# Kernel tuning notes

Hardware: AMD Instinct MI355X
Metric: run time of the kernel (lower is better)

The kernel has to match this reference:

```python
import jax, jax.numpy as jnp
import numpy as np

B, L, H, C, K, S = 32, 512, 336, 321, 8, 8   # batch, seq_len, pred_len, channels, leaders, states
FREQ = H // 2 + 1                            # 169
G = 2 * K + 1                                # filter groups
TEMP = 1.0
EPS = 1e-5


def setup_inputs() -> dict:
    key = jax.random.key(0)
    ks = jax.random.split(key, 12)
    x = jax.random.normal(ks[0], (B, L, C), jnp.float32)
    leader_ids = jax.random.randint(ks[1], (B, C, K), 0, C)
    shift = jax.random.randint(ks[2], (B, C, K), 0, L)
    r = jax.random.normal(ks[3], (B, C, K), jnp.float32)
    # backbone linear: seq_len -> pred_len
    Wb = jax.random.normal(ks[4], (H, L), jnp.float32) * float(1.0 / np.sqrt(L))
    bb = jnp.zeros((H,), jnp.float32)
    # factory classifier: (L + K) features -> state_num logits
    Wc = jax.random.normal(ks[5], (S, L + K), jnp.float32) * float(1.0 / np.sqrt(L + K))
    bc = jnp.zeros((S,), jnp.float32)
    # state prototype filters (complex, stored as re/im): [S, 2K+1, FREQ]
    states_re = jax.random.normal(ks[6], (S, G, FREQ), jnp.float32) * float(1.0 / np.sqrt(S))
    states_im = jax.random.normal(ks[7], (S, G, FREQ), jnp.float32) * float(1.0 / np.sqrt(S))
    # complex mix layer: 3*FREQ -> FREQ
    Wm_re = jax.random.normal(ks[8], (FREQ, 3 * FREQ), jnp.float32) * float(1.0 / np.sqrt(3 * FREQ))
    Wm_im = jax.random.normal(ks[9], (FREQ, 3 * FREQ), jnp.float32) * float(1.0 / np.sqrt(3 * FREQ))
    bm_re = jnp.zeros((FREQ,), jnp.float32)
    bm_im = jnp.zeros((FREQ,), jnp.float32)
    return dict(x=x, r=r, Wb=Wb, bb=bb, Wc=Wc, bc=bc,
                states_re=states_re, states_im=states_im,
                Wm_re=Wm_re, Wm_im=Wm_im, bm_re=bm_re, bm_im=bm_im,
                leader_ids=leader_ids, shift=shift)


def reference(x, r, Wb, bb, Wc, bc, states_re, states_im, Wm_re, Wm_im, bm_re, bm_im, leader_ids, shift):
    xc = jnp.transpose(x, (0, 2, 1))                      # [B,C,L]
    mu = xc.mean(-1, keepdims=True)
    norm = jnp.sqrt(xc.var(-1, keepdims=True) + EPS)
    xn = (xc - mu) / norm                                 # instance_norm
    y_hat = jnp.einsum('bcl,hl->bch', xn, Wb) + bb        # backbone [B,C,H]

    # --- shifted_leader_seq (torch.no_grad) ---
    full = jax.lax.stop_gradient(jnp.concatenate([xn, y_hat], -1))      # [B,C,L+H]
    lead_full = full[jnp.arange(B)[:, None, None], leader_ids]          # [B,C,K,L+H]
    t_idx = (L - shift)[..., None] + jnp.arange(H)                      # [B,C,K,H]
    seq_shifted = jnp.take_along_axis(lead_full, t_idx, axis=-1)        # [B,C,K,H]
    r = jax.lax.stop_gradient(r)

    # softmax leader weights with leading constant-one slot
    ones = jnp.ones((B, C, 1), xn.dtype)
    r_soft = jax.nn.softmax(jnp.concatenate([ones, jnp.abs(r)], -1) / TEMP, axis=-1)  # [B,C,K+1]

    # --- factory: state-mixed complex filters ---
    feat = jnp.concatenate([xn, r_soft[..., 1:]], -1)                   # [B,C,L+K]
    p = jax.nn.softmax(jnp.einsum('bcf,sf->bcs', feat, Wc) + bc, axis=-1)
    states = states_re + 1j * states_im                                 # [S,G,FREQ]
    filters = jnp.einsum('bcs,sgf->bcgf', p, states)                    # [B,C,2K+1,FREQ]

    # --- FFT filter multiply-sum + inverse FFT mix ---
    y_hat_f = jnp.fft.rfft(y_hat)                                       # [B,C,FREQ]
    seq_shifted_f = jnp.fft.rfft(seq_shifted) * filters[:, :, :K]       # [B,C,K,FREQ]
    seq_diff_f = (seq_shifted_f - y_hat_f[:, :, None]) * filters[:, :, K:-1]
    yh_f = y_hat_f * filters[:, :, -1]
    z = jnp.concatenate([seq_shifted_f.sum(2), seq_diff_f.sum(2), yh_f], -1)  # [B,C,3*FREQ]
    Wm = Wm_re + 1j * Wm_im
    mixed = jnp.einsum('bcf,gf->bcg', z, Wm) + (bm_re + 1j * bm_im)     # [B,C,FREQ]
    y_hat = y_hat + jnp.fft.irfft(mixed, n=H)

    y = y_hat * norm + mu
    return jnp.transpose(y, (0, 2, 1))                                  # [B,H,C]
```

## Files before the change

kernel.cpp:

```cpp
#include <hip/hip_runtime.h>
#include <math.h>

#define B_ 32
#define L_ 512
#define H_ 336
#define C_ 321
#define K_ 8
#define S_ 8
#define FREQ_ 169
#define G_ 17
#define LHB_ 848
#define F_FEAT 520
#define EPS_ 1e-5f
#define BCN_ (B_ * C_)
#define NROW_ (BCN_ * 9)
#define NROWP_ 92480
#define ZNBC_ 8

#ifndef M_PIf
#define M_PIf 3.14159265358979323846f
#endif

typedef __attribute__((ext_vector_type(8))) short short8v;
typedef __attribute__((ext_vector_type(4))) float f32x4;

__device__ __forceinline__ unsigned short f2bf(float x) {
    unsigned u = __builtin_bit_cast(unsigned, x);
    u += 0x7FFFu + ((u >> 16) & 1u);
    return (unsigned short)(u >> 16);
}
__device__ __forceinline__ float bf2f(unsigned short h) {
    return __builtin_bit_cast(float, (unsigned)h << 16);
}


__global__ void k_prep_dft(unsigned short* __restrict__ T) {
    int blk = blockIdx.x, kc = blk / 22, nt = blk % 22, lane = threadIdx.x;
    int n = nt * 16 + (lane & 15);
    int kb = kc * 32 + (lane >> 4) * 8;
    int f = n >> 1;
    unsigned short* dst = T + (size_t)blk * 512 + lane * 8;
    for (int i = 0; i < 8; ++i) {
        int k = kb + i;
        float val = 0.f;
        if (k < H_ && n < 2 * FREQ_) {
            int m = (k * f) % H_;
            float s, c;
            sincosf((float)m * (2.0f * M_PIf / (float)H_), &s, &c);
            val = (n & 1) ? -s : c;
        }
        dst[i] = f2bf(val);
    }
}

__global__ __launch_bounds__(256) void k_prep_tab(float* __restrict__ ctb,
                                                  float* __restrict__ stb) {
    int idx = blockIdx.x * 256 + threadIdx.x;
    if (idx >= FREQ_ * H_) return;
    int g = idx / H_, h = idx % H_;
    int m = (g * h) % H_;
    float s, c;
    sincosf((float)m * (2.0f * M_PIf / (float)H_), &s, &c);
    float wgt = ((g == 0 || g == FREQ_ - 1) ? 1.0f : 2.0f) * (1.0f / (float)H_);
    ctb[idx] = wgt * c;
    stb[idx] = -wgt * s;
}

__global__ __launch_bounds__(256) void k_prep_wt3(const float* __restrict__ Wm_re,
                                                  const float* __restrict__ Wm_im,
                                                  const float* __restrict__ ctb,
                                                  const float* __restrict__ stb,
                                                  unsigned short* __restrict__ T) {
    int t = blockIdx.x * 256 + threadIdx.x;
    if (t >= 512 * H_) return;
    int k = t / H_, h = t - k * H_;
    float s1 = 0.f, s2 = 0.f;
    if (k < 3 * FREQ_) {
        #pragma unroll 4
        for (int g = 0; g < FREQ_; ++g) {
            float ct = ctb[g * H_ + h];
            float st = stb[g * H_ + h];
            float wr = Wm_re[(size_t)g * (3 * FREQ_) + k];
            float wi = Wm_im[(size_t)g * (3 * FREQ_) + k];
            s1 += wr * ct + wi * st;
            s2 += wr * st - wi * ct;
        }
    }
    int nt = h >> 4, nr = h & 15;
    {
        int kc = k >> 5, kr = k & 31;
        int lane = ((kr >> 3) << 4) | nr;
        T[((size_t)(kc * 21 + nt)) * 512 + lane * 8 + (k & 7)] = f2bf(s1);
    }
    {
        int kk = k + 512;
        int kc = kk >> 5, kr = kk & 31;
        int lane = ((kr >> 3) << 4) | nr;
        T[((size_t)(kc * 21 + nt)) * 512 + lane * 8 + (kk & 7)] = f2bf(s2);
    }
}

__global__ __launch_bounds__(64) void k_prep_bv(const float* __restrict__ bm_re,
                                                const float* __restrict__ bm_im,
                                                const float* __restrict__ ctb,
                                                const float* __restrict__ stb,
                                                float* __restrict__ bvec) {
    int h = blockIdx.x * 64 + threadIdx.x;
    if (h >= H_) return;
    float acc = 0.f;
    for (int g = 0; g < FREQ_; ++g)
        acc += bm_re[g] * ctb[g * H_ + h] + bm_im[g] * stb[g * H_ + h];
    bvec[h] = acc;
}

__global__ void k_prep_wb(const float* __restrict__ Wb, unsigned short* __restrict__ T) {
    int blk = blockIdx.x, kc = blk / 21, nt = blk % 21, lane = threadIdx.x;
    int n = nt * 16 + (lane & 15);
    int kb = kc * 32 + (lane >> 4) * 8;
    unsigned short* dst = T + (size_t)blk * 512 + lane * 8;
    for (int i = 0; i < 8; ++i) {
        int k = kb + i;
        dst[i] = f2bf(Wb[(size_t)n * L_ + k]);
    }
}

__global__ __launch_bounds__(256) void k_prep_st2(const float* __restrict__ st_re,
                                                  const float* __restrict__ st_im,
                                                  float4* __restrict__ stf4,
                                                  float2* __restrict__ stg3) {
    int idx = blockIdx.x * 256 + threadIdx.x;
    if (idx < 64 * FREQ_) {
        int row = idx / FREQ_, f = idx % FREQ_;
        int k = row >> 3, s = row & 7;
        size_t b1 = (size_t)s * (G_ * FREQ_) + (size_t)k * FREQ_ + f;
        size_t b2 = (size_t)s * (G_ * FREQ_) + (size_t)(8 + k) * FREQ_ + f;
        stf4[idx] = make_float4(st_re[b1], st_im[b1], st_re[b2], st_im[b2]);
    }
    if (idx < 8 * FREQ_) {
        int s = idx / FREQ_, f = idx % FREQ_;
        size_t b3 = (size_t)s * (G_ * FREQ_) + (size_t)16 * FREQ_ + f;
        stg3[idx] = make_float2(st_re[b3], st_im[b3]);
    }
}

__global__ __launch_bounds__(256) void k_stats_part(const float* __restrict__ x,
                                                    float2* __restrict__ part) {
    __shared__ float red_s[4][64], red_q[4][64];
    int tid = threadIdx.x, w = tid >> 6, lane = tid & 63;
    int b = blockIdx.y, c0 = blockIdx.x * 64, l0 = blockIdx.z * 64;
    int c = c0 + lane;
    bool valid = (c < C_);
    const float* xb = x + ((size_t)b * L_) * C_;
    float s = 0.f, q = 0.f;
    for (int li = w; li < 64; li += 4) {
        float v = valid ? xb[(size_t)(l0 + li) * C_ + c] : 0.f;
        s += v; q += v * v;
    }
    red_s[w][lane] = s; red_q[w][lane] = q;
    __syncthreads();
    if (w == 0) {
        float S = red_s[0][lane] + red_s[1][lane] + red_s[2][lane] + red_s[3][lane];
        float Q = red_q[0][lane] + red_q[1][lane] + red_q[2][lane] + red_q[3][lane];
        part[(size_t)(((b * 6 + blockIdx.x) * 8) + blockIdx.z) * 64 + lane] = make_float2(S, Q);
    }
}

__global__ __launch_bounds__(256) void k_stats_fin(const float2* __restrict__ part,
                                                   float* __restrict__ muv,
                                                   float* __restrict__ nrm) {
    int t = blockIdx.x * 256 + threadIdx.x;
    int b = t / 384, rem = t % 384;
    int ct = rem / 64, cl = rem % 64;
    int c = ct * 64 + cl;
    if (b >= B_ || c >= C_) return;
    float S = 0.f, Q = 0.f;
    #pragma unroll
    for (int ls = 0; ls < 8; ++ls) {
        float2 p = part[(size_t)(((b * 6 + ct) * 8) + ls) * 64 + cl];
        S += p.x; Q += p.y;
    }
    float mu = S / (float)L_;
    float var = Q / (float)L_ - mu * mu;
    float n = sqrtf(var + EPS_);
    muv[(size_t)b * C_ + c] = mu;
    nrm[(size_t)b * C_ + c] = n;
}

__global__ __launch_bounds__(256) void k_norm(const float* __restrict__ x,
                                              const float* __restrict__ muv,
                                              const float* __restrict__ nrm,
                                              unsigned short* __restrict__ fullbf) {
    __shared__ float tl[64][65];
    int tid = threadIdx.x, w = tid >> 6, lane = tid & 63;
    int b = blockIdx.y, c0 = blockIdx.x * 64, l0 = blockIdx.z * 64;
    int c = c0 + lane;
    bool valid = (c < C_);
    const float* xb = x + ((size_t)b * L_) * C_;
    float mu = valid ? muv[(size_t)b * C_ + c] : 0.f;
    float inv = valid ? (1.0f / nrm[(size_t)b * C_ + c]) : 0.f;
    for (int li = w; li < 64; li += 4) {
        float v = valid ? xb[(size_t)(l0 + li) * C_ + c] : 0.f;
        tl[li][lane] = (v - mu) * inv;
    }
    __syncthreads();
    for (int cr = w; cr < 64; cr += 4) {
        int cc = c0 + cr;
        if (cc < C_ && lane < 32) {
            size_t bc = (size_t)b * C_ + cc;
            unsigned pk = (unsigned)f2bf(tl[2 * lane][cr]) |
                          ((unsigned)f2bf(tl[2 * lane + 1][cr]) << 16);
            ((unsigned*)fullbf)[(bc * LHB_ + l0) / 2 + lane] = pk;
        }
    }
}

__global__ __launch_bounds__(256) void k_yhat(const unsigned short* __restrict__ fullbf_r,
                                              const unsigned short* __restrict__ Wbsw,
                                              const float* __restrict__ bb,
                                              unsigned short* __restrict__ fullbf_w,
                                              float* __restrict__ yhf) {
    int bc0 = blockIdx.x * 32;
    int half = blockIdx.y;
    int tid = threadIdx.x, w = tid >> 6, lane = tid & 63;
    const int NTB0[5] = {0, 3, 6, 9, 11};
    const int NTB1[5] = {11, 14, 17, 19, 21};
    int nt0 = half ? NTB1[w] : NTB0[w];
    int ntn = (half ? NTB1[w + 1] : NTB0[w + 1]) - nt0;
    int r15 = lane & 15, kg = lane >> 4;
    f32x4 acc[2][3];
    #pragma unroll
    for (int mf = 0; mf < 2; ++mf)
        #pragma unroll
        for (int j = 0; j < 3; ++j) acc[mf][j] = (f32x4){0.f, 0.f, 0.f, 0.f};
    for (int kc = 0; kc < 16; ++kc) {
        short8v a[2];
        #pragma unroll
        for (int mf = 0; mf < 2; ++mf)
            a[mf] = *(const short8v*)(fullbf_r + ((size_t)(bc0 + mf * 16 + r15) * LHB_ + kc * 32 + kg * 8));
        #pragma unroll
        for (int j = 0; j < 3; ++j) {
            if (j >= ntn) continue;
            short8v bfr = *(const short8v*)(Wbsw + ((size_t)(kc * 21 + nt0 + j) * 512 + lane * 8));
            #pragma unroll
            for (int mf = 0; mf < 2; ++mf)
                acc[mf][j] = __builtin_amdgcn_mfma_f32_16x16x32_bf16(a[mf], bfr, acc[mf][j], 0, 0, 0);
        }
    }
    #pragma unroll
    for (int mf = 0; mf < 2; ++mf)
        #pragma unroll
        for (int j = 0; j < 3; ++j) {
            if (j >= ntn) continue;
            int n_ = (nt0 + j) * 16 + r15;
            #pragma unroll
            for (int reg = 0; reg < 4; ++reg) {
                int bc = bc0 + mf * 16 + kg * 4 + reg;
                float v = acc[mf][j][reg] + bb[n_];
                fullbf_w[(size_t)bc * LHB_ + L_ + n_] = f2bf(v);
                yhf[(size_t)bc * H_ + n_] = v;
            }
        }
}

__global__ __launch_bounds__(256) void k_p2(const unsigned short* __restrict__ fullbf,
                                            const float* __restrict__ r,
                                            const float* __restrict__ Wc,
                                            const float* __restrict__ bcv,
                                            float* __restrict__ p_out) {
    __shared__ float WcS[8 * F_FEAT];
    __shared__ float rsS[16][8];
    __shared__ float bcS[8];
    int tid = threadIdx.x, w = tid >> 6, lane = tid & 63;
    int bc0 = blockIdx.x * 16;
    for (int i = tid; i < 8 * F_FEAT; i += 256) WcS[i] = Wc[i];
    if (tid < 8) bcS[tid] = bcv[tid];
    if (tid < 16) {
        int bc = bc0 + tid;
        const float* rr = r + (size_t)bc * K_;
        float a[8]; float m = 1.0f;
        #pragma unroll
        for (int k = 0; k < 8; ++k) { a[k] = fabsf(rr[k]); m = fmaxf(m, a[k]); }
        float Z = expf(1.0f - m);
        float e[8];
        #pragma unroll
        for (int k = 0; k < 8; ++k) { e[k] = expf(a[k] - m); Z += e[k]; }
        float inv = 1.0f / Z;
        #pragma unroll
        for (int k = 0; k < 8; ++k) rsS[tid][k] = e[k] * inv;
    }
    __syncthreads();

    for (int i = 0; i < 4; ++i) {
        int bcl = w * 4 + i;
        int bc = bc0 + bcl;
        const unsigned* xrow = (const unsigned*)(fullbf + (size_t)bc * LHB_);
        float acc[8] = {0.f, 0.f, 0.f, 0.f, 0.f, 0.f, 0.f, 0.f};
        #pragma unroll
        for (int t = 0; t < 4; ++t) {
            int j = lane + t * 64;
            unsigned v = xrow[j];
            float x0 = bf2f((unsigned short)(v & 0xffff));
            float x1 = bf2f((unsigned short)(v >> 16));
            #pragma unroll
            for (int s = 0; s < 8; ++s)
                acc[s] += x0 * WcS[s * F_FEAT + 2 * j] + x1 * WcS[s * F_FEAT + 2 * j + 1];
        }
        if (lane < 8) {
            float xf = rsS[bcl][lane];
            #pragma unroll
            for (int s = 0; s < 8; ++s) acc[s] += xf * WcS[s * F_FEAT + L_ + lane];
        }
        #pragma unroll
        for (int s = 0; s < 8; ++s) {
            #pragma unroll
            for (int off = 32; off > 0; off >>= 1) acc[s] += __shfl_down(acc[s], off);
        }
        if (lane == 0) {
            float m = -1e30f;
            #pragma unroll
            for (int s = 0; s < 8; ++s) { acc[s] += bcS[s]; m = fmaxf(m, acc[s]); }
            float Z = 0.f; float e[8];
            #pragma unroll
            for (int s = 0; s < 8; ++s) { e[s] = expf(acc[s] - m); Z += e[s]; }
            float inv = 1.0f / Z;
            #pragma unroll
            for (int s = 0; s < 8; ++s) p_out[(size_t)bc * 8 + s] = e[s] * inv;
        }
    }
}

__global__ __launch_bounds__(512) void k_dft3(const unsigned short* __restrict__ fullbf,
                                              const int* __restrict__ leader,
                                              const int* __restrict__ shiftp,
                                              const unsigned short* __restrict__ Tsw,
                                              unsigned short* __restrict__ Xbf) {
    __shared__ unsigned short A[64 * 360];
    int tid = threadIdx.x, w = tid >> 6, lane = tid & 63;
    int row0 = blockIdx.x * 64;

    #pragma unroll
    for (int i = 0; i < 8; ++i) {
        int rr = w * 8 + i;
        int r = row0 + rr;
        unsigned short* dst = A + rr * 360;
        if (r < NROW_) {
            int bc = r / 9, k = r - bc * 9;
            int b = bc / C_;
            const unsigned short* src;
            if (k < 8) {
                int lead = leader[(size_t)bc * K_ + k];
                int sh = shiftp[(size_t)bc * K_ + k];
                src = fullbf + ((size_t)b * C_ + lead) * LHB_ + (L_ - sh);
            } else {
                src = fullbf + (size_t)bc * LHB_ + L_;
            }
            #pragma unroll
            for (int t = 0; t < 6; ++t) {
                int j = lane + t * 64;
                if (j < 352) dst[j] = (j < H_) ? src[j] : (unsigned short)0;
            }
        } else {
            #pragma unroll
            for (int t = 0; t < 6; ++t) {
                int j = lane + t * 64;
                if (j < 352) dst[j] = 0;
            }
        }
    }
    __syncthreads();

    const int NTB[9] = {0, 3, 6, 9, 11, 14, 17, 20, 22};
    int nt0 = NTB[w], ntn = NTB[w + 1] - nt0;
    int r15 = lane & 15, kg = lane >> 4;
    f32x4 acc[4][3];
    #pragma unroll
    for (int mf = 0; mf < 4; ++mf)
        #pragma unroll
        for (int j = 0; j < 3; ++j) acc[mf][j] = (f32x4){0.f, 0.f, 0.f, 0.f};
    for (int kc = 0; kc < 11; ++kc) {
        short8v a[4];
        #pragma unroll
        for (int mf = 0; mf < 4; ++mf)
            a[mf] = *(const short8v*)(A + (size_t)(mf * 16 + r15) * 360 + kc * 32 + kg * 8);
        #pragma unroll
        for (int j = 0; j < 3; ++j) {
            if (j >= ntn) continue;
            short8v bfr = *(const short8v*)(Tsw + ((size_t)(kc * 22 + nt0 + j) * 512 + lane * 8));
            #pragma unroll
            for (int mf = 0; mf < 4; ++mf)
                acc[mf][j] = __builtin_amdgcn_mfma_f32_16x16x32_bf16(a[mf], bfr, acc[mf][j], 0, 0, 0);
        }
    }
    #pragma unroll
    for (int mf = 0; mf < 4; ++mf)
        #pragma unroll
        for (int j = 0; j < 3; ++j) {
            if (j >= ntn) continue;
            int col = (nt0 + j) * 16 + r15;
            #pragma unroll
            for (int reg = 0; reg < 4; ++reg) {
                int row = row0 + mf * 16 + kg * 4 + reg;
                Xbf[(size_t)row * 352 + col] = f2bf(acc[mf][j][reg]);
            }
        }
}

__global__ __launch_bounds__(256) void k_z3(const unsigned* __restrict__ X32,
                                            const float* __restrict__ pbuf,
                                            const float4* __restrict__ stf4,
                                            const float2* __restrict__ stg3,
                                            unsigned short* __restrict__ zbf) {
    __shared__ float psL[ZNBC_][8];
    int tid = threadIdx.x;
    int bc0 = blockIdx.x * ZNBC_;
    if (tid < ZNBC_ * 8) {
        int bcl = tid >> 3, s = tid & 7;
        psL[bcl][s] = pbuf[(size_t)(bc0 + bcl) * 8 + s];
    }
    __syncthreads();

    if (tid < FREQ_) {
        int f = tid;
        float z1r[ZNBC_], z1i[ZNBC_], z2r[ZNBC_], z2i[ZNBC_], Yr[ZNBC_], Yi[ZNBC_];
        #pragma unroll
        for (int bcl = 0; bcl < ZNBC_; ++bcl) {
            z1r[bcl] = z1i[bcl] = z2r[bcl] = z2i[bcl] = 0.f;
            unsigned v = X32[((size_t)(bc0 + bcl) * 9 + 8) * 176 + f];
            Yr[bcl] = bf2f((unsigned short)(v & 0xffff));
            Yi[bcl] = bf2f((unsigned short)(v >> 16));
        }
        for (int k = 0; k < 8; ++k) {
            float4 stv[8];
            #pragma unroll
            for (int s = 0; s < 8; ++s) stv[s] = stf4[(size_t)(k * 8 + s) * FREQ_ + f];
            #pragma unroll
            for (int bcl = 0; bcl < ZNBC_; ++bcl) {
                float f1r = 0.f, f1i = 0.f, f2r = 0.f, f2i = 0.f;
                #pragma unroll
                for (int s = 0; s < 8; ++s) {
                    float p = psL[bcl][s];
                    f1r += p * stv[s].x; f1i += p * stv[s].y;
                    f2r += p * stv[s].z; f2i += p * stv[s].w;
                }
                unsigned v = X32[((size_t)(bc0 + bcl) * 9 + k) * 176 + f];
                float Xr = bf2f((unsigned short)(v & 0xffff));
                float Xi = bf2f((unsigned short)(v >> 16));
                float ar = Xr * f1r - Xi * f1i;
                float ai = Xr * f1i + Xi * f1r;
                z1r[bcl] += ar; z1i[bcl] += ai;
                float dr = ar - Yr[bcl], di = ai - Yi[bcl];
                z2r[bcl] += dr * f2r - di * f2i;
                z2i[bcl] += dr * f2i + di * f2r;
            }
        }
        #pragma unroll
        for (int bcl = 0; bcl < ZNBC_; ++bcl) {
            int bc = bc0 + bcl;
            float f3r = 0.f, f3i = 0.f;
            #pragma unroll
            for (int s = 0; s < 8; ++s) {
                float2 v3 = stg3[(size_t)s * FREQ_ + f];
                float p = psL[bcl][s];
                f3r += p * v3.x; f3i += p * v3.y;
            }
            unsigned short* zrow = zbf + (size_t)bc * 1024;
            zrow[f]       = f2bf(z1r[bcl]);  zrow[512 + f]       = f2bf(z1i[bcl]);
            zrow[169 + f] = f2bf(z2r[bcl]);  zrow[512 + 169 + f] = f2bf(z2i[bcl]);
            zrow[338 + f] = f2bf(Yr[bcl] * f3r - Yi[bcl] * f3i);
            zrow[512 + 338 + f] = f2bf(Yr[bcl] * f3i + Yi[bcl] * f3r);
        }
    } else if (tid >= 176 && tid < 176 + ZNBC_ * 10) {
        int t = tid - 176;
        int bcl = t / 10, o = t - bcl * 10;
        unsigned short* zrow = zbf + (size_t)(bc0 + bcl) * 1024;
        if (o < 5) zrow[507 + o] = 0;
        else       zrow[1019 + (o - 5)] = 0;
    }
}

__global__ __launch_bounds__(256) void k_mixf(const unsigned short* __restrict__ zbf,
                                              const unsigned short* __restrict__ WTsw,
                                              const float* __restrict__ bvec,
                                              const float* __restrict__ yhf,
                                              const float* __restrict__ muv,
                                              const float* __restrict__ nrm,
                                              float* __restrict__ ytmp) {
    int bc0 = blockIdx.x * 32;
    int half = blockIdx.y;
    int tid = threadIdx.x, w = tid >> 6, lane = tid & 63;
    const int NTB0[5] = {0, 3, 6, 9, 11};
    const int NTB1[5] = {11, 14, 17, 19, 21};
    int nt0 = half ? NTB1[w] : NTB0[w];
    int ntn = (half ? NTB1[w + 1] : NTB0[w + 1]) - nt0;
    int r15 = lane & 15, kg = lane >> 4;
    f32x4 acc[2][3];
    #pragma unroll
    for (int mf = 0; mf < 2; ++mf)
        #pragma unroll
        for (int j = 0; j < 3; ++j) acc[mf][j] = (f32x4){0.f, 0.f, 0.f, 0.f};
    for (int kc = 0; kc < 32; ++kc) {
        short8v a[2];
        #pragma unroll
        for (int mf = 0; mf < 2; ++mf)
            a[mf] = *(const short8v*)(zbf + ((size_t)(bc0 + mf * 16 + r15) * 1024 + kc * 32 + kg * 8));
        #pragma unroll
        for (int j = 0; j < 3; ++j) {
            if (j >= ntn) continue;
            short8v bfr = *(const short8v*)(WTsw + ((size_t)(kc * 21 + nt0 + j) * 512 + lane * 8));
            #pragma unroll
            for (int mf = 0; mf < 2; ++mf)
                acc[mf][j] = __builtin_amdgcn_mfma_f32_16x16x32_bf16(a[mf], bfr, acc[mf][j], 0, 0, 0);
        }
    }
    #pragma unroll
    for (int mf = 0; mf < 2; ++mf)
        #pragma unroll
        for (int j = 0; j < 3; ++j) {
            if (j >= ntn) continue;
            int h = (nt0 + j) * 16 + r15;
            float bv = bvec[h];
            #pragma unroll
            for (int reg = 0; reg < 4; ++reg) {
                int bc = bc0 + mf * 16 + kg * 4 + reg;
                float y = (yhf[(size_t)bc * H_ + h] + acc[mf][j][reg] + bv) * nrm[bc] + muv[bc];
                ytmp[(size_t)bc * H_ + h] = y;
            }
        }
}

__global__ __launch_bounds__(256) void k_out_t(const float* __restrict__ ytmp,
                                               float* __restrict__ out) {
    __shared__ float tile[32][33];
    int b = blockIdx.z;
    int h0 = blockIdx.x * 32, c0 = blockIdx.y * 32;
    int tx = threadIdx.x & 31, ty = threadIdx.x >> 5;
    #pragma unroll
    for (int i = 0; i < 4; ++i) {
        int cc = c0 + ty + i * 8, hh = h0 + tx;
        if (cc < C_ && hh < H_)
            tile[ty + i * 8][tx] = ytmp[((size_t)b * C_ + cc) * H_ + hh];
    }
    __syncthreads();
    #pragma unroll
    for (int i = 0; i < 4; ++i) {
        int hh = h0 + ty + i * 8, cc = c0 + tx;
        if (cc < C_ && hh < H_)
            out[((size_t)b * H_ + hh) * C_ + cc] = tile[tx][ty + i * 8];
    }
}

extern "C" void kernel_launch(void* const* d_in, const int* in_sizes, int n_in,
                              void* d_out, int out_size, void* d_ws, size_t ws_size,
                              hipStream_t stream) {
    const float* x     = (const float*)d_in[0];
    const float* r     = (const float*)d_in[1];
    const float* Wb    = (const float*)d_in[2];
    const float* bb    = (const float*)d_in[3];
    const float* Wc    = (const float*)d_in[4];
    const float* bcv   = (const float*)d_in[5];
    const float* st_re = (const float*)d_in[6];
    const float* st_im = (const float*)d_in[7];
    const float* Wm_re = (const float*)d_in[8];
    const float* Wm_im = (const float*)d_in[9];
    const float* bm_re = (const float*)d_in[10];
    const float* bm_im = (const float*)d_in[11];
    const int* leader  = (const int*)d_in[12];
    const int* shiftp  = (const int*)d_in[13];
    float* out = (float*)d_out;

    char* w = (char*)d_ws;
    auto carve = [&](size_t bytes) {
        char* p = w;
        w += (bytes + 255) & ~(size_t)255;
        return (void*)p;
    };
    unsigned short* Tdft = (unsigned short*)carve((size_t)11 * 22 * 512 * 2);
    unsigned short* WTsw = (unsigned short*)carve((size_t)32 * 21 * 512 * 2);
    unsigned short* Wbsw = (unsigned short*)carve((size_t)16 * 21 * 512 * 2);
    float*          ctb  = (float*)carve((size_t)FREQ_ * H_ * 4);
    float*          stb  = (float*)carve((size_t)FREQ_ * H_ * 4);
    float*          bvec = (float*)carve((size_t)H_ * 4);
    float4*         stf4 = (float4*)carve((size_t)64 * FREQ_ * 16);
    float2*         stg3 = (float2*)carve((size_t)8 * FREQ_ * 8);
    float2*         part = (float2*)carve((size_t)B_ * 6 * 8 * 64 * 8);
    unsigned short* fullbf = (unsigned short*)carve((size_t)BCN_ * LHB_ * 2);
    float*          yhf  = (float*)carve((size_t)BCN_ * H_ * 4);
    float*          muv  = (float*)carve((size_t)BCN_ * 4);
    float*          nrm  = (float*)carve((size_t)BCN_ * 4);
    float*          pbuf = (float*)carve((size_t)BCN_ * 8 * 4);
    unsigned short* zbf  = (unsigned short*)carve((size_t)BCN_ * 1024 * 2);
    float*          ytmp = (float*)carve((size_t)BCN_ * H_ * 4);
    unsigned short* Xbf  = (unsigned short*)carve((size_t)NROWP_ * 352 * 2);

    hipLaunchKernelGGL(k_prep_dft, dim3(11 * 22), dim3(64), 0, stream, Tdft);
    hipLaunchKernelGGL(k_prep_tab, dim3((FREQ_ * H_ + 255) / 256), dim3(256), 0, stream, ctb, stb);
    hipLaunchKernelGGL(k_prep_wt3, dim3((512 * H_ + 255) / 256), dim3(256), 0, stream,
                       Wm_re, Wm_im, ctb, stb, WTsw);
    hipLaunchKernelGGL(k_prep_bv,  dim3((H_ + 63) / 64), dim3(64), 0, stream, bm_re, bm_im, ctb, stb, bvec);
    hipLaunchKernelGGL(k_prep_wb,  dim3(16 * 21), dim3(64), 0, stream, Wb, Wbsw);
    hipLaunchKernelGGL(k_prep_st2, dim3((64 * FREQ_ + 255) / 256), dim3(256), 0, stream,
                       st_re, st_im, stf4, stg3);
    hipLaunchKernelGGL(k_stats_part, dim3(6, 32, 8), dim3(256), 0, stream, x, part);
    hipLaunchKernelGGL(k_stats_fin, dim3(48), dim3(256), 0, stream, part, muv, nrm);
    hipLaunchKernelGGL(k_norm, dim3(6, 32, 8), dim3(256), 0, stream, x, muv, nrm, fullbf);
    hipLaunchKernelGGL(k_yhat, dim3(BCN_ / 32, 2), dim3(256), 0, stream, fullbf, Wbsw, bb, fullbf, yhf);
    hipLaunchKernelGGL(k_p2, dim3(BCN_ / 16), dim3(256), 0, stream, fullbf, r, Wc, bcv, pbuf);
    hipLaunchKernelGGL(k_dft3, dim3(NROWP_ / 64), dim3(512), 0, stream,
                       fullbf, leader, shiftp, Tdft, Xbf);
    hipLaunchKernelGGL(k_z3, dim3(BCN_ / ZNBC_), dim3(256), 0, stream,
                       (const unsigned*)Xbf, pbuf, stf4, stg3, zbf);
    hipLaunchKernelGGL(k_mixf, dim3(BCN_ / 32, 2), dim3(256), 0, stream,
                       zbf, WTsw, bvec, yhf, muv, nrm, ytmp);
    hipLaunchKernelGGL(k_out_t, dim3((H_ + 31) / 32, (C_ + 31) / 32, B_), dim3(256), 0, stream,
                       ytmp, out);
}
```

Measured before the change: 258.0 us.

## Fuse DFT with filter-mix stage and fold output transpose into mix kernel

Merges the batched DFT GEMM with the z-computation so spectra stay in shared memory instead of round-tripping through a large global Xbf buffer. Each block now handles 7 (b,c) pairs, which gives 63 of 64 rows and wastes one MFMA row. The separate transpose kernel is removed: the mix kernel stages results in a shared tile and writes the transposed output directly. These changes cut global traffic and launches, at the cost of more shared memory per block and output writes that are strided across channels.

```diff
diff --git a/kernel.cpp b/kernel.cpp
--- a/kernel.cpp
+++ b/kernel.cpp
@@ -13,9 +13,7 @@
 #define F_FEAT 520
 #define EPS_ 1e-5f
 #define BCN_ (B_ * C_)
-#define NROW_ (BCN_ * 9)
-#define NROWP_ 92480
-#define ZNBC_ 8
+#define DZB_ 7
 
 #ifndef M_PIf
 #define M_PIf 3.14159265358979323846f
@@ -329,22 +327,34 @@
     }
 }
 
-__global__ __launch_bounds__(512) void k_dft3(const unsigned short* __restrict__ fullbf,
-                                              const int* __restrict__ leader,
-                                              const int* __restrict__ shiftp,
-                                              const unsigned short* __restrict__ Tsw,
-                                              unsigned short* __restrict__ Xbf) {
+__global__ __launch_bounds__(512) void k_dftz2(const unsigned short* __restrict__ fullbf,
+                                               const int* __restrict__ leader,
+                                               const int* __restrict__ shiftp,
+                                               const unsigned short* __restrict__ Tsw,
+                                               const float* __restrict__ pbuf,
+                                               const float4* __restrict__ stf4,
+                                               const float2* __restrict__ stg3,
+                                               unsigned short* __restrict__ zbf) {
     __shared__ unsigned short A[64 * 360];
+    __shared__ float psL[DZB_][8];
     int tid = threadIdx.x, w = tid >> 6, lane = tid & 63;
-    int row0 = blockIdx.x * 64;
+    int bc0 = blockIdx.x * DZB_;
+    unsigned* A32 = (unsigned*)A;
+    for (int i = tid; i < 64 * 180; i += 512) A32[i] = 0;
+    if (tid < DZB_ * 8) {
+        int bcl = tid >> 3, s = tid & 7;
+        int bc = bc0 + bcl;
+        psL[bcl][s] = (bc < BCN_) ? pbuf[(size_t)bc * 8 + s] : 0.f;
+    }
+    __syncthreads();
 
     #pragma unroll
     for (int i = 0; i < 8; ++i) {
         int rr = w * 8 + i;
-        int r = row0 + rr;
-        unsigned short* dst = A + rr * 360;
-        if (r < NROW_) {
-            int bc = r / 9, k = r - bc * 9;
+        if (rr >= 63) break;
+        int bcl = rr / 9, k = rr - bcl * 9;
+        int bc = bc0 + bcl;
+        if (bc < BCN_) {
             int b = bc / C_;
             const unsigned short* src;
             if (k < 8) {
@@ -354,16 +364,11 @@
             } else {
                 src = fullbf + (size_t)bc * LHB_ + L_;
             }
+            unsigned short* dst = A + rr * 360;
             #pragma unroll
             for (int t = 0; t < 6; ++t) {
                 int j = lane + t * 64;
-                if (j < 352) dst[j] = (j < H_) ? src[j] : (unsigned short)0;
-            }
-        } else {
-            #pragma unroll
-            for (int t = 0; t < 6; ++t) {
-                int j = lane + t * 64;
-                if (j < 352) dst[j] = 0;
+                if (j < H_) dst[j] = src[j];
             }
         }
     }
@@ -391,6 +396,8 @@
                 acc[mf][j] = __builtin_amdgcn_mfma_f32_16x16x32_bf16(a[mf], bfr, acc[mf][j], 0, 0, 0);
         }
     }
+    __syncthreads();
+
     #pragma unroll
     for (int mf = 0; mf < 4; ++mf)
         #pragma unroll
@@ -399,42 +406,34 @@
             int col = (nt0 + j) * 16 + r15;
             #pragma unroll
             for (int reg = 0; reg < 4; ++reg) {
-                int row = row0 + mf * 16 + kg * 4 + reg;
-                Xbf[(size_t)row * 352 + col] = f2bf(acc[mf][j][reg]);
+                int row = mf * 16 + kg * 4 + reg;
+                A[row * 360 + col] = f2bf(acc[mf][j][reg]);
             }
         }
-}
-
-__global__ __launch_bounds__(256) void k_z3(const unsigned* __restrict__ X32,
-                                            const float* __restrict__ pbuf,
-                                            const float4* __restrict__ stf4,
-                                            const float2* __restrict__ stg3,
-                                            unsigned short* __restrict__ zbf) {
-    __shared__ float psL[ZNBC_][8];
-    int tid = threadIdx.x;
-    int bc0 = blockIdx.x * ZNBC_;
-    if (tid < ZNBC_ * 8) {
-        int bcl = tid >> 3, s = tid & 7;
-        psL[bcl][s] = pbuf[(size_t)(bc0 + bcl) * 8 + s];
-    }
-    __syncthreads();
-
-    if (tid < FREQ_) {
-        int f = tid;
-        float z1r[ZNBC_], z1i[ZNBC_], z2r[ZNBC_], z2i[ZNBC_], Yr[ZNBC_], Yi[ZNBC_];
-        #pragma unroll
-        for (int bcl = 0; bcl < ZNBC_; ++bcl) {
-            z1r[bcl] = z1i[bcl] = z2r[bcl] = z2i[bcl] = 0.f;
-            unsigned v = X32[((size_t)(bc0 + bcl) * 9 + 8) * 176 + f];
-            Yr[bcl] = bf2f((unsigned short)(v & 0xffff));
-            Yi[bcl] = bf2f((unsigned short)(v >> 16));
+    __syncthreads();
+
+    if (tid < 338) {
+        int g = (tid >= 169) ? 1 : 0;
+        int f = tid - g * 169;
+        int bclo = g * 4;
+        int nb = g ? 3 : 4;
+        float z1r[4], z1i[4], z2r[4], z2i[4], Yr[4], Yi[4];
+        #pragma unroll
+        for (int bl = 0; bl < 4; ++bl) {
+            z1r[bl] = z1i[bl] = z2r[bl] = z2i[bl] = 0.f;
+            int row = (bclo + bl) * 9 + 8;
+            unsigned v = (bl < nb) ? A32[row * 180 + f] : 0u;
+            Yr[bl] = bf2f((unsigned short)(v & 0xffff));
+            Yi[bl] = bf2f((unsigned short)(v >> 16));
         }
         for (int k = 0; k < 8; ++k) {
             float4 stv[8];
             #pragma unroll
             for (int s = 0; s < 8; ++s) stv[s] = stf4[(size_t)(k * 8 + s) * FREQ_ + f];
             #pragma unroll
-            for (int bcl = 0; bcl < ZNBC_; ++bcl) {
+            for (int bl = 0; bl < 4; ++bl) {
+                if (bl >= nb) continue;
+                int bcl = bclo + bl;
                 float f1r = 0.f, f1i = 0.f, f2r = 0.f, f2i = 0.f;
                 #pragma unroll
                 for (int s = 0; s < 8; ++s) {
@@ -442,20 +441,23 @@
                     f1r += p * stv[s].x; f1i += p * stv[s].y;
                     f2r += p * stv[s].z; f2i += p * stv[s].w;
                 }
-                unsigned v = X32[((size_t)(bc0 + bcl) * 9 + k) * 176 + f];
+                unsigned v = A32[(bcl * 9 + k) * 180 + f];
                 float Xr = bf2f((unsigned short)(v & 0xffff));
                 float Xi = bf2f((unsigned short)(v >> 16));
                 float ar = Xr * f1r - Xi * f1i;
                 float ai = Xr * f1i + Xi * f1r;
-                z1r[bcl] += ar; z1i[bcl] += ai;
-                float dr = ar - Yr[bcl], di = ai - Yi[bcl];
-                z2r[bcl] += dr * f2r - di * f2i;
-                z2i[bcl] += dr * f2i + di * f2r;
+                z1r[bl] += ar; z1i[bl] += ai;
+                float dr = ar - Yr[bl], di = ai - Yi[bl];
+                z2r[bl] += dr * f2r - di * f2i;
+                z2i[bl] += dr * f2i + di * f2r;
             }
         }
         #pragma unroll
-        for (int bcl = 0; bcl < ZNBC_; ++bcl) {
+        for (int bl = 0; bl < 4; ++bl) {
+            if (bl >= nb) continue;
+            int bcl = bclo + bl;
             int bc = bc0 + bcl;
+            if (bc >= BCN_) continue;
             float f3r = 0.f, f3i = 0.f;
             #pragma unroll
             for (int s = 0; s < 8; ++s) {
@@ -464,27 +466,31 @@
                 f3r += p * v3.x; f3i += p * v3.y;
             }
             unsigned short* zrow = zbf + (size_t)bc * 1024;
-            zrow[f]       = f2bf(z1r[bcl]);  zrow[512 + f]       = f2bf(z1i[bcl]);
-            zrow[169 + f] = f2bf(z2r[bcl]);  zrow[512 + 169 + f] = f2bf(z2i[bcl]);
-            zrow[338 + f] = f2bf(Yr[bcl] * f3r - Yi[bcl] * f3i);
-            zrow[512 + 338 + f] = f2bf(Yr[bcl] * f3i + Yi[bcl] * f3r);
-        }
-    } else if (tid >= 176 && tid < 176 + ZNBC_ * 10) {
-        int t = tid - 176;
+            zrow[f]       = f2bf(z1r[bl]);  zrow[512 + f]       = f2bf(z1i[bl]);
+            zrow[169 + f] = f2bf(z2r[bl]);  zrow[512 + 169 + f] = f2bf(z2i[bl]);
+            zrow[338 + f] = f2bf(Yr[bl] * f3r - Yi[bl] * f3i);
+            zrow[512 + 338 + f] = f2bf(Yr[bl] * f3i + Yi[bl] * f3r);
+        }
+    } else if (tid >= 344 && tid < 344 + DZB_ * 10) {
+        int t = tid - 344;
         int bcl = t / 10, o = t - bcl * 10;
-        unsigned short* zrow = zbf + (size_t)(bc0 + bcl) * 1024;
-        if (o < 5) zrow[507 + o] = 0;
-        else       zrow[1019 + (o - 5)] = 0;
-    }
-}
-
-__global__ __launch_bounds__(256) void k_mixf(const unsigned short* __restrict__ zbf,
-                                              const unsigned short* __restrict__ WTsw,
-                                              const float* __restrict__ bvec,
-                                              const float* __restrict__ yhf,
-                                              const float* __restrict__ muv,
-                                              const float* __restrict__ nrm,
-                                              float* __restrict__ ytmp) {
+        int bc = bc0 + bcl;
+        if (bc < BCN_) {
+            unsigned short* zrow = zbf + (size_t)bc * 1024;
+            if (o < 5) zrow[507 + o] = 0;
+            else       zrow[1019 + (o - 5)] = 0;
+        }
+    }
+}
+
+__global__ __launch_bounds__(256) void k_mixf2(const unsigned short* __restrict__ zbf,
+                                               const unsigned short* __restrict__ WTsw,
+                                               const float* __restrict__ bvec,
+                                               const float* __restrict__ yhf,
+                                               const float* __restrict__ muv,
+                                               const float* __restrict__ nrm,
+                                               float* __restrict__ out) {
+    __shared__ float ytile[32][177];
     int bc0 = blockIdx.x * 32;
     int half = blockIdx.y;
     int tid = threadIdx.x, w = tid >> 6, lane = tid & 63;
@@ -492,6 +498,8 @@
     const int NTB1[5] = {11, 14, 17, 19, 21};
     int nt0 = half ? NTB1[w] : NTB0[w];
     int ntn = (half ? NTB1[w + 1] : NTB0[w + 1]) - nt0;
+    int h0 = half ? 176 : 0;
+    int hn = half ? 160 : 176;
     int r15 = lane & 15, kg = lane >> 4;
     f32x4 acc[2][3];
     #pragma unroll
@@ -521,31 +529,18 @@
             float bv = bvec[h];
             #pragma unroll
             for (int reg = 0; reg < 4; ++reg) {
-                int bc = bc0 + mf * 16 + kg * 4 + reg;
+                int bcl = mf * 16 + kg * 4 + reg;
+                int bc = bc0 + bcl;
                 float y = (yhf[(size_t)bc * H_ + h] + acc[mf][j][reg] + bv) * nrm[bc] + muv[bc];
-                ytmp[(size_t)bc * H_ + h] = y;
+                ytile[bcl][h - h0] = y;
             }
         }
-}
-
-__global__ __launch_bounds__(256) void k_out_t(const float* __restrict__ ytmp,
-                                               float* __restrict__ out) {
-    __shared__ float tile[32][33];
-    int b = blockIdx.z;
-    int h0 = blockIdx.x * 32, c0 = blockIdx.y * 32;
-    int tx = threadIdx.x & 31, ty = threadIdx.x >> 5;
-    #pragma unroll
-    for (int i = 0; i < 4; ++i) {
-        int cc = c0 + ty + i * 8, hh = h0 + tx;
-        if (cc < C_ && hh < H_)
-            tile[ty + i * 8][tx] = ytmp[((size_t)b * C_ + cc) * H_ + hh];
-    }
-    __syncthreads();
-    #pragma unroll
-    for (int i = 0; i < 4; ++i) {
-        int hh = h0 + ty + i * 8, cc = c0 + tx;
-        if (cc < C_ && hh < H_)
-            out[((size_t)b * H_ + hh) * C_ + cc] = tile[tx][ty + i * 8];
+    __syncthreads();
+    for (int idx = tid; idx < 32 * hn; idx += 256) {
+        int bcl = idx & 31, hrel = idx >> 5;
+        int bc = bc0 + bcl;
+        int b = bc / C_, c = bc - b * C_;
+        out[((size_t)b * H_ + h0 + hrel) * C_ + c] = ytile[bcl][hrel];
     }
 }
 
@@ -589,8 +584,6 @@
     float*          nrm  = (float*)carve((size_t)BCN_ * 4);
     float*          pbuf = (float*)carve((size_t)BCN_ * 8 * 4);
     unsigned short* zbf  = (unsigned short*)carve((size_t)BCN_ * 1024 * 2);
-    float*          ytmp = (float*)carve((size_t)BCN_ * H_ * 4);
-    unsigned short* Xbf  = (unsigned short*)carve((size_t)NROWP_ * 352 * 2);
 
     hipLaunchKernelGGL(k_prep_dft, dim3(11 * 22), dim3(64), 0, stream, Tdft);
     hipLaunchKernelGGL(k_prep_tab, dim3((FREQ_ * H_ + 255) / 256), dim3(256), 0, stream, ctb, stb);
@@ -605,12 +598,8 @@
     hipLaunchKernelGGL(k_norm, dim3(6, 32, 8), dim3(256), 0, stream, x, muv, nrm, fullbf);
     hipLaunchKernelGGL(k_yhat, dim3(BCN_ / 32, 2), dim3(256), 0, stream, fullbf, Wbsw, bb, fullbf, yhf);
     hipLaunchKernelGGL(k_p2, dim3(BCN_ / 16), dim3(256), 0, stream, fullbf, r, Wc, bcv, pbuf);
-    hipLaunchKernelGGL(k_dft3, dim3(NROWP_ / 64), dim3(512), 0, stream,
-                       fullbf, leader, shiftp, Tdft, Xbf);
-    hipLaunchKernelGGL(k_z3, dim3(BCN_ / ZNBC_), dim3(256), 0, stream,
-                       (const unsigned*)Xbf, pbuf, stf4, stg3, zbf);
-    hipLaunchKernelGGL(k_mixf, dim3(BCN_ / 32, 2), dim3(256), 0, stream,
-                       zbf, WTsw, bvec, yhf, muv, nrm, ytmp);
-    hipLaunchKernelGGL(k_out_t, dim3((H_ + 31) / 32, (C_ + 31) / 32, B_), dim3(256), 0, stream,
-                       ytmp, out);
-}
+    hipLaunchKernelGGL(k_dftz2, dim3((BCN_ + DZB_ - 1) / DZB_), dim3(512), 0, stream,
+                       fullbf, leader, shiftp, Tdft, pbuf, stf4, stg3, zbf);
+    hipLaunchKernelGGL(k_mixf2, dim3(BCN_ / 32, 2), dim3(256), 0, stream,
+                       zbf, WTsw, bvec, yhf, muv, nrm, out);
+}
```

After: 242.4 us. -6.0%, faster.
